# Kernel optimization log

Hardware: AMD Instinct MI355X
Metric: run time of the kernel (lower is better)

Reference implementation:

```python
import jax, jax.numpy as jnp
import numpy as np

N_ITERATIONS = 32
EPS = 1e-8


def setup_inputs() -> dict:
    key = jax.random.key(0)
    k1, k2 = jax.random.split(key)
    x = jax.random.normal(k1, (8, 1, 16384), dtype=jnp.float32)
    # learned dictionary, init uniform(-1, 1) as in the torch module
    d = jax.random.uniform(k2, (512, 1, 512), dtype=jnp.float32, minval=-1.0, maxval=1.0)
    return {"x": x, "d": d}


def reference(x, d):
    B, C, T = x.shape
    n_atoms, _, A = d.shape  # A = atom_size
    # unit_norm over (channels, atom_size) per atom
    dn = d / (jnp.sqrt(jnp.sum(d * d, axis=(1, 2), keepdims=True)) + EPS)
    batch_ids = jnp.arange(B)[:, None]
    offs = jnp.arange(A)[None, :]

    def step(carry, _):
        xr, recon = carry
        xp = jnp.pad(xr, ((0, 0), (0, 0), (0, A)))  # pad right by atom_size
        fm = jax.lax.conv_general_dilated(
            xp, dn, window_strides=(1,), padding='VALID',
            dimension_numbers=('NCH', 'OIH', 'NCH'))[..., :T]  # [B, n_atoms, T]
        flat = fm.reshape(B, n_atoms * T)
        values = jnp.max(flat, axis=-1)            # [B]
        indices = jnp.argmax(flat, axis=-1)        # [B]
        atom_idx = indices // T
        time_idx = indices % T
        atoms = dn[atom_idx] * values[:, None, None]  # [B, C, A]
        pos = time_idx[:, None] + offs                 # [B, A], max < T + A
        end = jnp.clip(time_idx + A, 0, T - 1)         # torch clamps end to T-1
        mask = pos < end[:, None]                      # [B, A]
        vals = jnp.where(mask[:, None, :], atoms, 0.0)  # [B, C, A]
        sp = jnp.zeros((B, C, T + A), xr.dtype)
        # positions are unique per batch item -> scatter-set into padded buffer
        sp = sp.at[batch_ids, :, pos].set(vals.transpose(0, 2, 1))
        sparse = sp[..., :T]
        return (xr - sparse, recon + sparse), None

    (residual, recon), _ = jax.lax.scan(step, (x, jnp.zeros_like(x)), None, length=N_ITERATIONS)
    return residual, recon
```

## Files before the change

### kernel.cpp

```cpp
#include <hip/hip_runtime.h>
#include <cstdint>

#define B_    8
#define T_    16384
#define NA_   512
#define A_    512
#define NIT_  32
#define EPSV  1e-8f

typedef unsigned long long u64;
typedef __attribute__((ext_vector_type(8))) short bf16x8;
typedef __attribute__((ext_vector_type(4))) float f32x4;

union Frag { uint4 u; bf16x8 f; };

#define OFF_INV   0
#define OFF_SELA  512
#define OFF_SELT  768
#define OFF_SELV  1024
#define OFF_CM    1280
#define OFF_RMA   2098432
#define OFF_RMB   2106624
#define OFF_XRA   2114816
#define OFF_XRB   2245888
#define OFF_DPK   2376960
#define MAIN_NEED 2639104
#define OFF_BAR   2639104
#define PERS_NEED (OFF_BAR + 4096)
#define OFF_SXR   OFF_CM
#define OFF_SCAND (OFF_CM + 131072)
#define S_NEED    (OFF_SCAND + 16)

__device__ __forceinline__ unsigned int encf(float f) {
    unsigned int u = __float_as_uint(f);
    return (u & 0x80000000u) ? ~u : (u | 0x80000000u);
}
__device__ __forceinline__ float decf(unsigned int e) {
    unsigned int u = (e & 0x80000000u) ? (e & 0x7fffffffu) : ~e;
    return __uint_as_float(u);
}
__device__ __forceinline__ u64 umax64(u64 a, u64 b) { return a > b ? a : b; }
__device__ __forceinline__ u64 enc64(float v, unsigned int flat) {
    return (((u64)encf(v)) << 32) | (unsigned int)~flat;
}
__device__ __forceinline__ u64 shfl_xor_u64(u64 v, int mask) {
    unsigned int lo = (unsigned int)v, hi = (unsigned int)(v >> 32);
    lo = __shfl_xor(lo, mask, 64);
    hi = __shfl_xor(hi, mask, 64);
    return (((u64)hi) << 32) | lo;
}
__device__ __forceinline__ u64 shfl_down_u64(u64 v, int off) {
    unsigned int lo = (unsigned int)v, hi = (unsigned int)(v >> 32);
    lo = __shfl_down(lo, off, 64);
    hi = __shfl_down(hi, off, 64);
    return (((u64)hi) << 32) | lo;
}
__device__ __forceinline__ unsigned short f2bf(float v) {
    unsigned int u = __float_as_uint(v);
    return (unsigned short)((u + 0x7fffu + ((u >> 16) & 1u)) >> 16);
}
__device__ __forceinline__ unsigned int packhl(float v) {
    unsigned short hb = f2bf(v);
    unsigned short lb = f2bf(v - __uint_as_float((unsigned int)hb << 16));
    return (unsigned int)hb | ((unsigned int)lb << 16);
}

__device__ __forceinline__ float ld_af(const float* p) {
    return __hip_atomic_load(p, __ATOMIC_RELAXED, __HIP_MEMORY_SCOPE_AGENT);
}
__device__ __forceinline__ void st_af(float* p, float v) {
    __hip_atomic_store(p, v, __ATOMIC_RELAXED, __HIP_MEMORY_SCOPE_AGENT);
}
__device__ __forceinline__ u64 ld_au64(const u64* p) {
    return __hip_atomic_load(p, __ATOMIC_RELAXED, __HIP_MEMORY_SCOPE_AGENT);
}
__device__ __forceinline__ void st_au64(u64* p, u64 v) {
    __hip_atomic_store(p, v, __ATOMIC_RELAXED, __HIP_MEMORY_SCOPE_AGENT);
}

__device__ __forceinline__ void b_barrier(unsigned int* slots, int ag, unsigned int gen) {
    __syncthreads();
    const int tid = threadIdx.x;
    if (tid == 0)
        __hip_atomic_store(&slots[ag << 4], gen, __ATOMIC_RELAXED, __HIP_MEMORY_SCOPE_AGENT);
    if (tid < 64) {
        const unsigned int* sp = &slots[(tid & 31) << 4];
        int spins = 0;
        while (__hip_atomic_load(sp, __ATOMIC_RELAXED, __HIP_MEMORY_SCOPE_AGENT) < gen) {
            __builtin_amdgcn_s_sleep(1);
            if (++spins > (1 << 20)) break;
        }
    }
    __syncthreads();
    asm volatile("" ::: "memory");
}

__device__ __forceinline__ void run_super(const uint4* bhp, const uint4* blp,
                                          const uint4* Adl, int sw,
                                          int c0, int tbase, int chbase,
                                          u64* cml, const float* ivv,
                                          int a0, int q, int cl) {
    const int base = c0 << 4;
    f32x4 acc[8];
    const f32x4 zero = {0.f, 0.f, 0.f, 0.f};
    #pragma unroll
    for (int g = 0; g < 8; ++g) acc[g] = zero;

    Frag bh[8], bl[8];
    #pragma unroll
    for (int pp = 0; pp < 8; ++pp) {
        bh[pp].u = bhp[base + 4 * pp];
        bl[pp].u = blp[base + 4 * pp];
    }
    for (int js0 = 0; js0 < 32; js0 += 8) {
        #pragma unroll
        for (int ju = 0; ju < 8; ++ju) {
            const int js = js0 + ju;
            Frag Af;
            Af.u = Adl[(q + 4 * js) ^ sw];
            #pragma unroll
            for (int g = 0; g < 8; ++g)
                acc[g] = __builtin_amdgcn_mfma_f32_16x16x32_bf16(Af.f, bh[(g + ju) & 7].f, acc[g], 0, 0, 0);
            #pragma unroll
            for (int g = 0; g < 8; ++g)
                acc[g] = __builtin_amdgcn_mfma_f32_16x16x32_bf16(Af.f, bl[(g + ju) & 7].f, acc[g], 0, 0, 0);
            bh[ju].u = bhp[base + 4 * (js + 8)];
            bl[ju].u = blp[base + 4 * (js + 8)];
        }
    }
    #pragma unroll
    for (int r = 0; r < 4; ++r) {
        const int atom4 = 4 * q + r;
        const int atom = a0 + atom4;
        u64 m0 = 0ull, m1 = 0ull;
        #pragma unroll
        for (int g = 0; g < 4; ++g) {
            int t = tbase + 64 * c0 + 16 * g + cl;
            m0 = umax64(m0, enc64(acc[g][r] * ivv[r], (unsigned int)(atom * T_ + t)));
        }
        #pragma unroll
        for (int g = 4; g < 8; ++g) {
            int t = tbase + 64 * c0 + 16 * g + cl;
            m1 = umax64(m1, enc64(acc[g][r] * ivv[r], (unsigned int)(atom * T_ + t)));
        }
        m0 = umax64(m0, shfl_xor_u64(m0, 1));
        m0 = umax64(m0, shfl_xor_u64(m0, 2));
        m0 = umax64(m0, shfl_xor_u64(m0, 4));
        m0 = umax64(m0, shfl_xor_u64(m0, 8));
        m1 = umax64(m1, shfl_xor_u64(m1, 1));
        m1 = umax64(m1, shfl_xor_u64(m1, 2));
        m1 = umax64(m1, shfl_xor_u64(m1, 4));
        m1 = umax64(m1, shfl_xor_u64(m1, 8));
        if (cl == 0) {
            cml[(atom4 << 8) + chbase + c0] = m0;
            cml[(atom4 << 8) + chbase + c0 + 1] = m1;
        }
    }
}

__device__ __forceinline__ void run_single(const uint4* bhp, const uint4* blp,
                                           const uint4* Adl, int sw,
                                           int c, int tbase, int chbase,
                                           u64* cml, const float* ivv,
                                           int a0, int q, int cl) {
    const int base = c << 4;
    f32x4 acc[4];
    const f32x4 zero = {0.f, 0.f, 0.f, 0.f};
    #pragma unroll
    for (int g = 0; g < 4; ++g) acc[g] = zero;

    Frag bh[4], bl[4];
    #pragma unroll
    for (int pp = 0; pp < 4; ++pp) {
        bh[pp].u = bhp[base + 4 * pp];
        bl[pp].u = blp[base + 4 * pp];
    }
    for (int js0 = 0; js0 < 32; js0 += 4) {
        #pragma unroll
        for (int ju = 0; ju < 4; ++ju) {
            const int js = js0 + ju;
            Frag Af;
            Af.u = Adl[(q + 4 * js) ^ sw];
            #pragma unroll
            for (int g = 0; g < 4; ++g)
                acc[g] = __builtin_amdgcn_mfma_f32_16x16x32_bf16(Af.f, bh[(g + ju) & 3].f, acc[g], 0, 0, 0);
            #pragma unroll
            for (int g = 0; g < 4; ++g)
                acc[g] = __builtin_amdgcn_mfma_f32_16x16x32_bf16(Af.f, bl[(g + ju) & 3].f, acc[g], 0, 0, 0);
            bh[ju].u = bhp[base + 4 * (js + 4)];
            bl[ju].u = blp[base + 4 * (js + 4)];
        }
    }
    #pragma unroll
    for (int r = 0; r < 4; ++r) {
        const int atom4 = 4 * q + r;
        const int atom = a0 + atom4;
        u64 m0 = 0ull;
        #pragma unroll
        for (int g = 0; g < 4; ++g) {
            int t = tbase + 64 * c + 16 * g + cl;
            m0 = umax64(m0, enc64(acc[g][r] * ivv[r], (unsigned int)(atom * T_ + t)));
        }
        m0 = umax64(m0, shfl_xor_u64(m0, 1));
        m0 = umax64(m0, shfl_xor_u64(m0, 2));
        m0 = umax64(m0, shfl_xor_u64(m0, 4));
        m0 = umax64(m0, shfl_xor_u64(m0, 8));
        if (cl == 0)
            cml[(atom4 << 8) + chbase + c] = m0;
    }
}

__global__ __launch_bounds__(64) void k_inv(const float* __restrict__ d, float* __restrict__ inv,
                                            unsigned int* __restrict__ bar) {
    const int a = blockIdx.x, lane = threadIdx.x;
    if (bar && a == 0) {
        for (int i = lane; i < 4096; i += 64) bar[i] = 0u;
    }
    const float* row = d + a * A_;
    float s = 0.f;
    for (int i = lane; i < A_; i += 64) { float v = row[i]; s = fmaf(v, v, s); }
    #pragma unroll
    for (int o = 32; o > 0; o >>= 1) s += __shfl_down(s, o, 64);
    if (lane == 0) inv[a] = 1.0f / (sqrtf(s) + EPSV);
}

__global__ __launch_bounds__(256) void k_split_d(const float* __restrict__ d,
                                                 unsigned int* __restrict__ dpk) {
    int id = blockIdx.x * 256 + threadIdx.x;
    dpk[id] = packhl(d[id]);
}

__global__ __launch_bounds__(512) void k_persist(const float* __restrict__ x,
                                                 float* __restrict__ xrA,
                                                 float* __restrict__ xrB,
                                                 const float* __restrict__ d,
                                                 const float* __restrict__ inv,
                                                 u64* __restrict__ rmW,
                                                 int* __restrict__ selA,
                                                 int* __restrict__ selT,
                                                 float* __restrict__ selV,
                                                 unsigned int* __restrict__ bar,
                                                 float* __restrict__ out) {
    __shared__ u64 red16[16];
    __shared__ int   selAL[NIT_];
    __shared__ int   selTL[NIT_];
    __shared__ float selVL[NIT_];
    __shared__ uint4 s_hh[4][410];
    __shared__ uint4 s_ll[4][410];
    __shared__ uint4 dl4[16 * 128];
    __shared__ u64  cml[16 * 256];
    const int ag = blockIdx.x, b = blockIdx.y, tid = threadIdx.x;
    const int wave = tid >> 6, lane = tid & 63;
    const int cl = lane & 15, q = lane >> 4;
    const int a0 = ag * 16;
    unsigned int* slots = bar + (b << 9);

    {
        const float4* gsrc = (const float4*)(d + (a0 << 9));
        #pragma unroll
        for (int s = 0; s < 4; ++s) {
            int i = tid + 512 * s;
            int row = i >> 7, c4 = i & 127;
            float4 f = gsrc[i];
            uint4 pk;
            pk.x = packhl(f.x);
            pk.y = packhl(f.y);
            pk.z = packhl(f.z);
            pk.w = packhl(f.w);
            dl4[(row << 7) | (c4 ^ (row & 7))] = pk;
        }
    }

    const uint4* Adl = dl4 + (cl << 7);
    const int sw = cl & 7;
    float ivv[4];
    #pragma unroll
    for (int r = 0; r < 4; ++r) ivv[r] = inv[a0 + 4 * q + r];
    const uint4* bhp = &s_hh[cl & 3][(cl >> 2) + q];
    const uint4* blp = &s_ll[cl & 3][(cl >> 2) + q];
    unsigned int* hw = (unsigned int*)s_hh;
    unsigned int* lw = (unsigned int*)s_ll;

    {
        const float* xb = x + b * T_;
        float cur[4], nxt[4];
        #pragma unroll
        for (int s = 0; s < 4; ++s) {
            const int e = tid + 512 * s;
            cur[s] = (e < 1539) ? xb[e] : 0.f;
        }
        for (int w = 0; w < 16; ++w) {
            const int wb = w << 10;
            if (w) __syncthreads();
            #pragma unroll
            for (int s = 0; s < 4; ++s) {
                const int e = tid + 512 * s;
                if (e < 1539) {
                    float xv = cur[s];
                    unsigned int pw = packhl(xv);
                    unsigned int hword = (pw & 0xffffu) * 0x10001u;
                    unsigned int lword = (pw >> 16) * 0x10001u;
                    #pragma unroll
                    for (int sh = 0; sh < 4; ++sh) {
                        int i = e - sh;
                        if (i >= 0 && i < 1536) { hw[sh * 1640 + i] = hword; lw[sh * 1640 + i] = lword; }
                    }
                }
            }
            __syncthreads();
            if (w + 1 < 16) {
                const int wb2 = (w + 1) << 10;
                #pragma unroll
                for (int s = 0; s < 4; ++s) {
                    const int e = tid + 512 * s;
                    const int t = wb2 + e;
                    nxt[s] = (e < 1539 && t < T_) ? xb[t] : 0.f;
                }
            }
            run_super(bhp, blp, Adl, sw, 2 * wave, wb, w << 4,
                      cml, ivv, a0, q, cl);
            #pragma unroll
            for (int s = 0; s < 4; ++s) cur[s] = nxt[s];
        }
    }
    __syncthreads();

    {
        #pragma unroll
        for (int rr = 0; rr < 2; ++rr) {
            const int rl = wave * 2 + rr;
            const u64* p = cml + (rl << 8);
            u64 m = umax64(umax64(p[lane], p[lane + 64]),
                           umax64(p[lane + 128], p[lane + 192]));
            #pragma unroll
            for (int o = 32; o > 0; o >>= 1) m = umax64(m, shfl_down_u64(m, o));
            if (lane == 0) red16[rl] = m;
        }
        __syncthreads();
        if (wave == 0) {
            u64 wv = (lane < 16) ? red16[lane] : 0ull;
            #pragma unroll
            for (int o = 8; o > 0; o >>= 1) wv = umax64(wv, shfl_xor_u64(wv, o));
            if (lane == 0) st_au64(&rmW[b * 32 + ag], wv);
        }
    }
    unsigned int gen = 1;
    b_barrier(slots, ag, gen); ++gen;

    for (int it = 0; it < NIT_; ++it) {
        const u64* rwp = rmW + ((it & 1) << 8) + b * 32;
        u64 am = ld_au64(&rwp[lane & 31]);
        #pragma unroll
        for (int o = 16; o > 0; o >>= 1) am = umax64(am, shfl_xor_u64(am, o));
        const unsigned int enc = (unsigned int)(am >> 32);
        const unsigned int flat = ~(unsigned int)am;
        const int asel = (int)((flat >> 14) & (NA_ - 1));
        const int tsel = (int)(flat & (T_ - 1));
        const float v = decf(enc);
        if (tid == 0) { selAL[it] = asel; selTL[it] = tsel; selVL[it] = v; }
        if (ag == 0 && tid == 0) {
            selA[it * B_ + b] = asel;
            selT[it * B_ + b] = tsel;
            selV[it * B_ + b] = v;
        }
        if (it == NIT_ - 1) break;
        const int L = min(A_, (T_ - 1) - tsel);
        const float vv = v * inv[asel];

        const float* xrPrev = (it == 0) ? x : ((it & 1) ? xrB : xrA);
        float*       xrNext = (it & 1) ? xrA : xrB;

        int ab = 0, nch = 0, NS = 0;
        float cbuf[4];
        if (L > 0) {
            const int tbeg = max(0, tsel - (A_ - 1));
            const int tend = tsel + L;
            ab = tbeg & ~63;
            const int ae = (tend + 63) & ~63;
            const int W = ae - ab;
            nch = W >> 6;
            NS = W + 512;
            #pragma unroll
            for (int s = 0; s < 4; ++s) {
                const int e = tid + 512 * s;
                const int t = ab + e;
                cbuf[s] = (e < NS + 3 && t < T_) ? ld_af(&xrPrev[b * T_ + t]) : 0.f;
            }
        }

        {
            int t = ag * 512 + tid;
            float xv = ld_af(&xrPrev[b * T_ + t]);
            int o = t - tsel;
            if (L > 0 && o >= 0 && o < L) xv = fmaf(-vv, d[asel * A_ + o], xv);
            st_af(&xrNext[b * T_ + t], xv);
        }

        if (L > 0) {
            #pragma unroll
            for (int s = 0; s < 4; ++s) {
                const int e = tid + 512 * s;
                if (e < NS + 3) {
                    float xv = cbuf[s];
                    int o = (ab + e) - tsel;
                    if (o >= 0 && o < L) xv = fmaf(-vv, d[asel * A_ + o], xv);
                    unsigned int pw = packhl(xv);
                    unsigned int hword = (pw & 0xffffu) * 0x10001u;
                    unsigned int lword = (pw >> 16) * 0x10001u;
                    #pragma unroll
                    for (int sh = 0; sh < 4; ++sh) {
                        int i = e - sh;
                        if (i >= 0 && i < NS) { hw[sh * 1640 + i] = hword; lw[sh * 1640 + i] = lword; }
                    }
                }
            }
            __syncthreads();

            {
                const int lo = (wave * nch) >> 3;
                const int hi = ((wave + 1) * nch) >> 3;
                int c = lo;
                for (; c + 1 < hi; c += 2)
                    run_super(bhp, blp, Adl, sw, c, ab, ab >> 6,
                              cml, ivv, a0, q, cl);
                if (c < hi)
                    run_single(bhp, blp, Adl, sw, c, ab, ab >> 6,
                               cml, ivv, a0, q, cl);
            }
            __syncthreads();
        }

        #pragma unroll
        for (int rr = 0; rr < 2; ++rr) {
            const int rl = wave * 2 + rr;
            const u64* p = cml + (rl << 8);
            u64 m = umax64(umax64(p[lane], p[lane + 64]),
                           umax64(p[lane + 128], p[lane + 192]));
            #pragma unroll
            for (int o = 32; o > 0; o >>= 1) m = umax64(m, shfl_down_u64(m, o));
            if (lane == 0) red16[rl] = m;
        }
        __syncthreads();
        if (wave == 0) {
            u64 wv = (lane < 16) ? red16[lane] : 0ull;
            #pragma unroll
            for (int o = 8; o > 0; o >>= 1) wv = umax64(wv, shfl_xor_u64(wv, o));
            if (lane == 0) st_au64(&rmW[(((it + 1) & 1) << 8) + b * 32 + ag], wv);
        }

        b_barrier(slots, ag, gen); ++gen;
    }

    __syncthreads();
    {
        const int t = ag * 512 + tid;
        const int gid = b * T_ + t;
        float r = x[gid];
        float rec = 0.f;
        for (int k = 0; k < NIT_; ++k) {
            int a  = selAL[k] & (NA_ - 1);
            int ts = selTL[k] & (T_ - 1);
            float vvl = selVL[k] * inv[a];
            int o = t - ts;
            int Lf = min(A_, (T_ - 1) - ts);
            if (o >= 0 && o < Lf) {
                float c = vvl * d[a * A_ + o];
                r -= c;
                rec += c;
            }
        }
        out[gid] = r;
        out[B_ * T_ + gid] = rec;
    }
}


__global__ __launch_bounds__(512) void k_conv(const float* __restrict__ x,
                                              const unsigned int* __restrict__ dpk,
                                              const float* __restrict__ inv,
                                              u64* __restrict__ cm,
                                              float* __restrict__ xrA) {
    __shared__ uint4 s_hh[4][202];
    __shared__ uint4 s_ll[4][202];
    const int tid = threadIdx.x;
    const int wave = tid >> 6, lane = tid & 63;
    const int cl = lane & 15, q = lane >> 4;
    const int wb = blockIdx.x * 256;
    const int gb = blockIdx.z;

    unsigned int* hw = (unsigned int*)s_hh;
    unsigned int* lw = (unsigned int*)s_ll;
    for (int e = tid; e < 776; e += 512) {
        int t = wb + e;
        float xv = (t < T_) ? x[gb * T_ + t] : 0.f;
        if (blockIdx.y == 0 && e < 256) xrA[gb * T_ + wb + e] = xv;
        unsigned int pw = packhl(xv);
        unsigned int hword = (pw & 0xffffu) * 0x10001u;
        unsigned int lword = (pw >> 16) * 0x10001u;
        #pragma unroll
        for (int s = 0; s < 4; ++s) {
            int i = e - s;
            if (i >= 0 && i < 772) { hw[s * 808 + i] = hword; lw[s * 808 + i] = lword; }
        }
    }
    __syncthreads();

    const int a_base = blockIdx.y * 128 + (wave & 1) * 64;
    const int t0l = (wave >> 1) * 64;
    const unsigned int* Ap[4];
    #pragma unroll
    for (int at = 0; at < 4; ++at)
        Ap[at] = dpk + ((a_base + 16 * at + cl) << 9) + 4 * q;
    const uint4* bhp = &s_hh[cl & 3][(t0l >> 2) + (cl >> 2) + q];
    const uint4* blp = &s_ll[cl & 3][(t0l >> 2) + (cl >> 2) + q];

    f32x4 acc[4][4];
    const f32x4 zero = {0.f, 0.f, 0.f, 0.f};
    #pragma unroll
    for (int at = 0; at < 4; ++at)
        #pragma unroll
        for (int tt = 0; tt < 4; ++tt) acc[at][tt] = zero;

    for (int j0 = 0; j0 < A_; j0 += 16) {
        Frag Af[4], bh[4], bl[4];
        #pragma unroll
        for (int at = 0; at < 4; ++at) Af[at].u = *(const uint4*)(Ap[at] + j0);
        #pragma unroll
        for (int tt = 0; tt < 4; ++tt) {
            bh[tt].u = bhp[4 * tt + (j0 >> 2)];
            bl[tt].u = blp[4 * tt + (j0 >> 2)];
        }
        #pragma unroll
        for (int tt = 0; tt < 4; ++tt)
            #pragma unroll
            for (int at = 0; at < 4; ++at)
                acc[at][tt] = __builtin_amdgcn_mfma_f32_16x16x32_bf16(Af[at].f, bh[tt].f, acc[at][tt], 0, 0, 0);
        #pragma unroll
        for (int tt = 0; tt < 4; ++tt)
            #pragma unroll
            for (int at = 0; at < 4; ++at)
                acc[at][tt] = __builtin_amdgcn_mfma_f32_16x16x32_bf16(Af[at].f, bl[tt].f, acc[at][tt], 0, 0, 0);
    }

    const int t0 = wb + t0l;
    const int ch = t0 >> 6;
    #pragma unroll
    for (int at = 0; at < 4; ++at) {
        #pragma unroll
        for (int r = 0; r < 4; ++r) {
            const int atom = a_base + 16 * at + 4 * q + r;
            const float iv = inv[atom];
            u64 m = 0ull;
            #pragma unroll
            for (int tt = 0; tt < 4; ++tt) {
                int t = t0 + 16 * tt + cl;
                m = umax64(m, enc64(acc[at][tt][r] * iv, (unsigned int)(atom * T_ + t)));
            }
            m = umax64(m, shfl_xor_u64(m, 1));
            m = umax64(m, shfl_xor_u64(m, 2));
            m = umax64(m, shfl_xor_u64(m, 4));
            m = umax64(m, shfl_xor_u64(m, 8));
            if (cl == 0)
                cm[((size_t)(gb * NA_ + atom) << 8) + ch] = m;
        }
    }
}

__global__ __launch_bounds__(256) void k_tables(const u64* __restrict__ cm, u64* __restrict__ rm) {
    const int row = blockIdx.x * 4 + (threadIdx.x >> 6);
    const int lane = threadIdx.x & 63;
    const u64* p = cm + ((size_t)row << 8);
    u64 m = 0ull;
    #pragma unroll
    for (int k = 0; k < 4; ++k) m = umax64(m, p[lane + 64 * k]);
    #pragma unroll
    for (int o = 32; o > 0; o >>= 1) m = umax64(m, shfl_down_u64(m, o));
    if (lane == 0) rm[row] = m;
}

__global__ __launch_bounds__(512) void k_it(const float* __restrict__ xrPrev,
                                            float* __restrict__ xrNext,
                                            const float* __restrict__ d,
                                            const float* __restrict__ inv,
                                            const unsigned int* __restrict__ dpk,
                                            u64* __restrict__ cm,
                                            const u64* __restrict__ rmPrev,
                                            u64* __restrict__ rmNext,
                                            int* __restrict__ selA,
                                            int* __restrict__ selT,
                                            float* __restrict__ selV,
                                            int it) {
    __shared__ u64 red8[8];
    __shared__ uint4 s_hh[4][410];
    __shared__ uint4 s_ll[4][410];
    __shared__ uint4 dl4[16 * 128];
    const int ag = blockIdx.x, b = blockIdx.y, tid = threadIdx.x;
    const int wave = tid >> 6, lane = tid & 63;
    const int cl = lane & 15, q = lane >> 4;
    const int a0 = ag * 16;

    {
        const uint4* gsrc = (const uint4*)(dpk + (a0 << 9));
        #pragma unroll
        for (int s = 0; s < 4; ++s) {
            int i = tid + 512 * s;
            int row = i >> 7, c4 = i & 127;
            dl4[(row << 7) | (c4 ^ (row & 7))] = gsrc[i];
        }
    }

    const u64* rp = rmPrev + b * NA_;
    u64 am = rp[tid];
    #pragma unroll
    for (int o = 32; o > 0; o >>= 1) am = umax64(am, shfl_xor_u64(am, o));
    if (lane == 0) red8[wave] = am;
    __syncthreads();
    u64 win = red8[0];
    #pragma unroll
    for (int w2 = 1; w2 < 8; ++w2) win = umax64(win, red8[w2]);
    const unsigned int enc = (unsigned int)(win >> 32);
    const unsigned int flat = ~(unsigned int)win;
    const int asel = (int)((flat >> 14) & (NA_ - 1));
    const int tsel = (int)(flat & (T_ - 1));
    const float v = decf(enc);
    if (ag == 0 && tid == 0) {
        selA[it * B_ + b] = asel;
        selT[it * B_ + b] = tsel;
        selV[it * B_ + b] = v;
    }
    const int L = min(A_, (T_ - 1) - tsel);
    const float vv = v * inv[asel];

    {
        int t = ag * 512 + tid;
        float xv = xrPrev[b * T_ + t];
        int o = t - tsel;
        if (L > 0 && o >= 0 && o < L) xv = fmaf(-vv, d[asel * A_ + o], xv);
        xrNext[b * T_ + t] = xv;
    }

    if (L > 0) {
        const int tbeg = max(0, tsel - (A_ - 1));
        const int tend = tsel + L;
        const int ab = tbeg & ~63;
        const int ae = (tend + 63) & ~63;
        const int W = ae - ab;
        const int nch = W >> 6;
        const int NS = W + 512;

        unsigned int* hw = (unsigned int*)s_hh;
        unsigned int* lw = (unsigned int*)s_ll;
        for (int e = tid; e < NS + 3; e += 512) {
            int t = ab + e;
            float xv = (t < T_) ? xrPrev[b * T_ + t] : 0.f;
            int o = t - tsel;
            if (o >= 0 && o < L) xv = fmaf(-vv, d[asel * A_ + o], xv);
            unsigned int pw = packhl(xv);
            unsigned int hword = (pw & 0xffffu) * 0x10001u;
            unsigned int lword = (pw >> 16) * 0x10001u;
            #pragma unroll
            for (int s = 0; s < 4; ++s) {
                int i = e - s;
                if (i >= 0 && i < NS) { hw[s * 1640 + i] = hword; lw[s * 1640 + i] = lword; }
            }
        }
        __syncthreads();

        const uint4* Adl = dl4 + (cl << 7);
        const int sw = cl & 7;
        float ivv[4];
        #pragma unroll
        for (int r = 0; r < 4; ++r) ivv[r] = inv[a0 + 4 * q + r];
        const uint4* bhp = &s_hh[cl & 3][(cl >> 2) + q];
        const uint4* blp = &s_ll[cl & 3][(cl >> 2) + q];

        for (int c = wave; c < nch; c += 8) {
            f32x4 acc[4];
            const f32x4 zero = {0.f, 0.f, 0.f, 0.f};
            #pragma unroll
            for (int tt = 0; tt < 4; ++tt) acc[tt] = zero;

            Frag bh[4], bl[4];
            #pragma unroll
            for (int pp = 0; pp < 4; ++pp) {
                bh[pp].u = bhp[16 * c + 4 * pp];
                bl[pp].u = blp[16 * c + 4 * pp];
            }
            for (int j0 = 0; j0 < A_; j0 += 64) {
                #pragma unroll
                for (int u = 0; u < 4; ++u) {
                    const int jj = j0 + 16 * u;
                    Frag Af;
                    Af.u = Adl[(q + (jj >> 2)) ^ sw];
                    #pragma unroll
                    for (int tt = 0; tt < 4; ++tt)
                        acc[tt] = __builtin_amdgcn_mfma_f32_16x16x32_bf16(Af.f, bh[(u + tt) & 3].f, acc[tt], 0, 0, 0);
                    #pragma unroll
                    for (int tt = 0; tt < 4; ++tt)
                        acc[tt] = __builtin_amdgcn_mfma_f32_16x16x32_bf16(Af.f, bl[(u + tt) & 3].f, acc[tt], 0, 0, 0);
                    bh[u].u = bhp[16 * c + (jj >> 2) + 16];
                    bl[u].u = blp[16 * c + (jj >> 2) + 16];
                }
            }
            #pragma unroll
            for (int r = 0; r < 4; ++r) {
                const int atom = a0 + 4 * q + r;
                u64 mm = 0ull;
                #pragma unroll
                for (int tt = 0; tt < 4; ++tt) {
                    int t = ab + 64 * c + 16 * tt + cl;
                    mm = umax64(mm, enc64(acc[tt][r] * ivv[r], (unsigned int)(atom * T_ + t)));
                }
                mm = umax64(mm, shfl_xor_u64(mm, 1));
                mm = umax64(mm, shfl_xor_u64(mm, 2));
                mm = umax64(mm, shfl_xor_u64(mm, 4));
                mm = umax64(mm, shfl_xor_u64(mm, 8));
                if (cl == 0)
                    cm[((size_t)(b * NA_ + atom) << 8) + (ab >> 6) + c] = mm;
            }
        }
        __syncthreads();
    }

    #pragma unroll
    for (int rr = 0; rr < 2; ++rr) {
        const int row = a0 + wave * 2 + rr;
        const u64* p = cm + ((size_t)(b * NA_ + row) << 8);
        u64 m = umax64(umax64(p[lane], p[lane + 64]),
                       umax64(p[lane + 128], p[lane + 192]));
        #pragma unroll
        for (int o = 32; o > 0; o >>= 1) m = umax64(m, shfl_down_u64(m, o));
        if (lane == 0) rmNext[b * NA_ + row] = m;
    }
}

__global__ void s_init(const float* __restrict__ x, float* __restrict__ xr,
                       u64* __restrict__ cand) {
    int i = blockIdx.x * 256 + threadIdx.x;
    if (i < B_ * T_) xr[i] = x[i];
    if (i < B_) cand[i] = 0ull;
}
__global__ __launch_bounds__(256) void s_scan(const float* __restrict__ xr,
                                              const float* __restrict__ d,
                                              const float* __restrict__ inv,
                                              u64* __restrict__ cand) {
    __shared__ float dLs[A_];
    __shared__ u64 redU[256];
    const int aB = blockIdx.x, b = blockIdx.y, tid = threadIdx.x;
    const float iv = inv[aB];
    for (int i = tid; i < A_; i += 256) dLs[i] = d[aB * A_ + i] * iv;
    __syncthreads();
    const float* xb = xr + b * T_;
    u64 best = 0ull;
    for (int t = tid; t < T_; t += 256) {
        float acc = 0.f;
        int lim = min(A_, T_ - t);
        for (int i = 0; i < lim; ++i) acc = fmaf(dLs[i], xb[t + i], acc);
        best = umax64(best, enc64(acc, (unsigned int)(aB * T_ + t)));
    }
    redU[tid] = best;
    __syncthreads();
    for (int s = 128; s > 0; s >>= 1) {
        if (tid < s) redU[tid] = umax64(redU[tid], redU[tid + s]);
        __syncthreads();
    }
    if (tid == 0) atomicMax(&cand[b], redU[0]);
}
__global__ void s_apply(float* __restrict__ xr, const float* __restrict__ d,
                        const float* __restrict__ inv, u64* __restrict__ cand,
                        int* selA, int* selT, float* selV, int it) {
    const int b = blockIdx.x, tid = threadIdx.x;
    u64 win = cand[b];
    unsigned int enc = (unsigned int)(win >> 32);
    unsigned int flat = ~(unsigned int)win;
    int a = (int)((flat >> 14) & (NA_ - 1)), t = (int)(flat & (T_ - 1));
    float v = decf(enc);
    if (tid == 0) { selA[it * B_ + b] = a; selT[it * B_ + b] = t; selV[it * B_ + b] = v; }
    float vvl = v * inv[a];
    int L = min(A_, (T_ - 1) - t);
    for (int o = tid; o < L; o += 256) xr[b * T_ + t + o] -= vvl * d[a * A_ + o];
    if (tid == 0) cand[b] = 0ull;
}

__global__ __launch_bounds__(256) void k_final(const float* __restrict__ x,
                                               const float* __restrict__ d,
                                               const int* __restrict__ selA,
                                               const int* __restrict__ selT,
                                               const float* __restrict__ selV,
                                               const float* __restrict__ inv,
                                               float* __restrict__ out) {
    const int gid = blockIdx.x * 256 + threadIdx.x;
    const int b = gid >> 14;
    const int t = gid & (T_ - 1);
    float r = x[gid];
    float rec = 0.f;
    for (int k = 0; k < NIT_; ++k) {
        int a  = selA[k * B_ + b] & (NA_ - 1);
        int ts = selT[k * B_ + b] & (T_ - 1);
        float vvl = selV[k * B_ + b] * inv[a];
        int o = t - ts;
        int L = min(A_, (T_ - 1) - ts);
        if (o >= 0 && o < L) {
            float c = vvl * d[a * A_ + o];
            r -= c;
            rec += c;
        }
    }
    out[gid] = r;
    out[B_ * T_ + gid] = rec;
}

extern "C" void kernel_launch(void* const* d_in, const int* in_sizes, int n_in,
                              void* d_out, int out_size, void* d_ws, size_t ws_size,
                              hipStream_t stream) {
    const float* x = (const float*)d_in[0];
    const float* d = (const float*)d_in[1];
    float* out = (float*)d_out;
    float* ws = (float*)d_ws;
    const size_t wsf = ws_size / sizeof(float);

    float* inv  = ws + OFF_INV;
    int*   selA = (int*)(ws + OFF_SELA);
    int*   selT = (int*)(ws + OFF_SELT);
    float* selV = ws + OFF_SELV;

    if (wsf < (size_t)S_NEED) return;

    const bool persistOK = wsf >= (size_t)PERS_NEED;
    unsigned int* bar = persistOK ? (unsigned int*)(ws + OFF_BAR) : (unsigned int*)0;

    k_inv<<<dim3(NA_), dim3(64), 0, stream>>>(d, inv, bar);

    if (wsf >= (size_t)MAIN_NEED) {
        u64* cm  = (u64*)(ws + OFF_CM);
        u64* rmA = (u64*)(ws + OFF_RMA);
        u64* rmB = (u64*)(ws + OFF_RMB);
        float* xrA = ws + OFF_XRA;
        float* xrB = ws + OFF_XRB;
        unsigned int* dpk = (unsigned int*)(ws + OFF_DPK);

        if (persistOK) {
            u64* rmW = (u64*)(ws + OFF_RMA);
            k_persist<<<dim3(NA_ / 16, B_), dim3(512), 0, stream>>>(x, xrA, xrB, d, inv,
                                                                    rmW, selA, selT, selV,
                                                                    bar, out);
            return;
        }

        k_split_d<<<dim3(NA_ * A_ / 256), dim3(256), 0, stream>>>(d, dpk);
        k_conv<<<dim3(T_ / 256, NA_ / 128, B_), dim3(512), 0, stream>>>(x, dpk, inv, cm, xrA);
        k_tables<<<dim3(B_ * NA_ / 4), dim3(256), 0, stream>>>(cm, rmA);
        for (int it = 0; it < NIT_; ++it) {
            const float* xp = (it & 1) ? xrB : xrA;
            float*       xn = (it & 1) ? xrA : xrB;
            const u64*   ro = (it & 1) ? rmB : rmA;
            u64*         rn = (it & 1) ? rmA : rmB;
            k_it<<<dim3(NA_ / 16, B_), dim3(512), 0, stream>>>(xp, xn, d, inv, dpk,
                                                               cm, ro, rn,
                                                               selA, selT, selV, it);
        }
    } else {
        float* xr = ws + OFF_SXR;
        u64* cand = (u64*)(ws + OFF_SCAND);
        s_init<<<dim3((B_ * T_ + 255) / 256), dim3(256), 0, stream>>>(x, xr, cand);
        for (int it = 0; it < NIT_; ++it) {
            s_scan<<<dim3(NA_, B_), dim3(256), 0, stream>>>(xr, d, inv, cand);
            s_apply<<<dim3(B_), dim3(256), 0, stream>>>(xr, d, inv, cand, selA, selT, selV, it);
        }
    }

    k_final<<<dim3(B_ * T_ / 256), dim3(256), 0, stream>>>(x, d, selA, selT, selV, inv, out);
}
```

Measured before the change: 811.2 us.

## Skip dictionary-low term in persistent correlation using separate high-part atom layout

In the persistent kernel's run_super and run_single, the second MFMA pass over the signal's low bf16 residual now multiplies only the dictionary's high bf16 part. It uses a compact half-K layout: a new ah4 shared array packs only the high halves of the dictionary, and an lp buffer holds just the signal's low halves, loaded as K=32 pairs. This roughly halves the MFMA work and LDS traffic of the low-part correction term. It drops the tiny low×low cross product, slightly changing numerics, and adds shared-memory layout complexity plus scalar 32-bit LDS loads that may cause bank conflicts.

Measured after the change: 706.4 us. 1.15x faster.

```diff
diff --git a/kernel.cpp b/kernel.cpp
--- a/kernel.cpp
+++ b/kernel.cpp
@@ -13,6 +13,8 @@
 typedef __attribute__((ext_vector_type(4))) float f32x4;
 
 union Frag { uint4 u; bf16x8 f; };
+
+#define MFMA16(a, b, c) __builtin_amdgcn_mfma_f32_16x16x32_bf16((a), (b), (c), 0, 0, 0)
 
 #define OFF_INV   0
 #define OFF_SELA  512
@@ -95,8 +97,17 @@
     asm volatile("" ::: "memory");
 }
 
-__device__ __forceinline__ void run_super(const uint4* bhp, const uint4* blp,
+__device__ __forceinline__ uint4 lp4(const unsigned int* lps, int w) {
+    uint4 r;
+    r.x = lps[w]; r.y = lps[w + 1]; r.z = lps[w + 2]; r.w = lps[w + 3];
+    return r;
+}
+
+
+__device__ __forceinline__ void run_super(const uint4* bhp,
                                           const uint4* Adl, int sw,
+                                          const unsigned int* lps,
+                                          const uint4* A2p,
                                           int c0, int tbase, int chbase,
                                           u64* cml, const float* ivv,
                                           int a0, int q, int cl) {
@@ -106,26 +117,40 @@
     #pragma unroll
     for (int g = 0; g < 8; ++g) acc[g] = zero;
 
-    Frag bh[8], bl[8];
-    #pragma unroll
-    for (int pp = 0; pp < 8; ++pp) {
-        bh[pp].u = bhp[base + 4 * pp];
-        bl[pp].u = blp[base + 4 * pp];
-    }
-    for (int js0 = 0; js0 < 32; js0 += 8) {
-        #pragma unroll
-        for (int ju = 0; ju < 8; ++ju) {
-            const int js = js0 + ju;
-            Frag Af;
-            Af.u = Adl[(q + 4 * js) ^ sw];
-            #pragma unroll
-            for (int g = 0; g < 8; ++g)
-                acc[g] = __builtin_amdgcn_mfma_f32_16x16x32_bf16(Af.f, bh[(g + ju) & 7].f, acc[g], 0, 0, 0);
-            #pragma unroll
-            for (int g = 0; g < 8; ++g)
-                acc[g] = __builtin_amdgcn_mfma_f32_16x16x32_bf16(Af.f, bl[(g + ju) & 7].f, acc[g], 0, 0, 0);
-            bh[ju].u = bhp[base + 4 * (js + 8)];
-            bl[ju].u = blp[base + 4 * (js + 8)];
+    {
+        Frag bh[8];
+        #pragma unroll
+        for (int pp = 0; pp < 8; ++pp) bh[pp].u = bhp[base + 4 * pp];
+        for (int js0 = 0; js0 < 32; js0 += 8) {
+            #pragma unroll
+            for (int ju = 0; ju < 8; ++ju) {
+                const int js = js0 + ju;
+                Frag Af;
+                Af.u = Adl[(q + 4 * js) ^ sw];
+                #pragma unroll
+                for (int g = 0; g < 8; ++g)
+                    acc[g] = MFMA16(Af.f, bh[(g + ju) & 7].f, acc[g]);
+                bh[ju].u = bhp[base + 4 * (js + 8)];
+            }
+        }
+    }
+    {
+        const int bb = 32 * c0 + 4 * q + (cl >> 1);
+        Frag b2[8];
+        #pragma unroll
+        for (int m = 0; m < 8; ++m) b2[m].u = lp4(lps, bb + 8 * m);
+        for (int j2b = 0; j2b < 4; ++j2b) {
+            #pragma unroll
+            for (int j2u = 0; j2u < 4; ++j2u) {
+                const int j2 = 4 * j2b + j2u;
+                Frag A2;
+                A2.u = A2p[(4 * j2 + q) ^ sw];
+                #pragma unroll
+                for (int g = 0; g < 8; ++g)
+                    acc[g] = MFMA16(A2.f, b2[(g + 2 * j2u) & 7].f, acc[g]);
+                b2[(2 * j2u) & 7].u     = lp4(lps, bb + 8 * (2 * j2 + 8));
+                b2[(2 * j2u + 1) & 7].u = lp4(lps, bb + 8 * (2 * j2 + 9));
+            }
         }
     }
     #pragma unroll
@@ -158,8 +183,10 @@
     }
 }
 
-__device__ __forceinline__ void run_single(const uint4* bhp, const uint4* blp,
+__device__ __forceinline__ void run_single(const uint4* bhp,
                                            const uint4* Adl, int sw,
+                                           const unsigned int* lps,
+                                           const uint4* A2p,
                                            int c, int tbase, int chbase,
                                            u64* cml, const float* ivv,
                                            int a0, int q, int cl) {
@@ -169,26 +196,40 @@
     #pragma unroll
     for (int g = 0; g < 4; ++g) acc[g] = zero;
 
-    Frag bh[4], bl[4];
-    #pragma unroll
-    for (int pp = 0; pp < 4; ++pp) {
-        bh[pp].u = bhp[base + 4 * pp];
-        bl[pp].u = blp[base + 4 * pp];
-    }
-    for (int js0 = 0; js0 < 32; js0 += 4) {
-        #pragma unroll
-        for (int ju = 0; ju < 4; ++ju) {
-            const int js = js0 + ju;
-            Frag Af;
-            Af.u = Adl[(q + 4 * js) ^ sw];
-            #pragma unroll
-            for (int g = 0; g < 4; ++g)
-                acc[g] = __builtin_amdgcn_mfma_f32_16x16x32_bf16(Af.f, bh[(g + ju) & 3].f, acc[g], 0, 0, 0);
-            #pragma unroll
-            for (int g = 0; g < 4; ++g)
-                acc[g] = __builtin_amdgcn_mfma_f32_16x16x32_bf16(Af.f, bl[(g + ju) & 3].f, acc[g], 0, 0, 0);
-            bh[ju].u = bhp[base + 4 * (js + 4)];
-            bl[ju].u = blp[base + 4 * (js + 4)];
+    {
+        Frag bh[4];
+        #pragma unroll
+        for (int pp = 0; pp < 4; ++pp) bh[pp].u = bhp[base + 4 * pp];
+        for (int js0 = 0; js0 < 32; js0 += 4) {
+            #pragma unroll
+            for (int ju = 0; ju < 4; ++ju) {
+                const int js = js0 + ju;
+                Frag Af;
+                Af.u = Adl[(q + 4 * js) ^ sw];
+                #pragma unroll
+                for (int g = 0; g < 4; ++g)
+                    acc[g] = MFMA16(Af.f, bh[(g + ju) & 3].f, acc[g]);
+                bh[ju].u = bhp[base + 4 * (js + 4)];
+            }
+        }
+    }
+    {
+        const int bb = 32 * c + 4 * q + (cl >> 1);
+        Frag b2[4];
+        #pragma unroll
+        for (int m = 0; m < 4; ++m) b2[m].u = lp4(lps, bb + 8 * m);
+        for (int j2b = 0; j2b < 8; ++j2b) {
+            #pragma unroll
+            for (int j2u = 0; j2u < 2; ++j2u) {
+                const int j2 = 2 * j2b + j2u;
+                Frag A2;
+                A2.u = A2p[(4 * j2 + q) ^ sw];
+                #pragma unroll
+                for (int g = 0; g < 4; ++g)
+                    acc[g] = MFMA16(A2.f, b2[(g + 2 * j2u) & 3].f, acc[g]);
+                b2[(2 * j2u) & 3].u     = lp4(lps, bb + 8 * (2 * j2 + 4));
+                b2[(2 * j2u + 1) & 3].u = lp4(lps, bb + 8 * (2 * j2 + 5));
+            }
         }
     }
     #pragma unroll
@@ -246,7 +287,8 @@
     __shared__ int   selTL[NIT_];
     __shared__ float selVL[NIT_];
     __shared__ uint4 s_hh[4][410];
-    __shared__ uint4 s_ll[4][410];
+    __shared__ unsigned int lp[2][816];
+    __shared__ uint4 ah4[16 * 64];
     __shared__ uint4 dl4[16 * 128];
     __shared__ u64  cml[16 * 256];
     const int ag = blockIdx.x, b = blockIdx.y, tid = threadIdx.x;
@@ -254,9 +296,12 @@
     const int cl = lane & 15, q = lane >> 4;
     const int a0 = ag * 16;
     unsigned int* slots = bar + (b << 9);
+    unsigned short* lp0s = (unsigned short*)&lp[0][0];
+    unsigned short* lp1s = (unsigned short*)&lp[1][0];
 
     {
         const float4* gsrc = (const float4*)(d + (a0 << 9));
+        unsigned int* ah32 = (unsigned int*)ah4;
         #pragma unroll
         for (int s = 0; s < 4; ++s) {
             int i = tid + 512 * s;
@@ -268,18 +313,25 @@
             pk.z = packhl(f.z);
             pk.w = packhl(f.w);
             dl4[(row << 7) | (c4 ^ (row & 7))] = pk;
+            unsigned int d0 = (pk.x & 0xffffu) | ((pk.y & 0xffffu) << 16);
+            unsigned int d1 = (pk.z & 0xffffu) | ((pk.w & 0xffffu) << 16);
+            int u = c4 >> 1;
+            int l0 = (2 * c4) & 3;
+            int abase = (row << 8) + ((u ^ (row & 7)) << 2);
+            ah32[abase + l0] = d0;
+            ah32[abase + l0 + 1] = d1;
         }
     }
 
     const uint4* Adl = dl4 + (cl << 7);
+    const uint4* A2p = ah4 + (cl << 6);
     const int sw = cl & 7;
+    const unsigned int* lps = &lp[cl & 1][0];
     float ivv[4];
     #pragma unroll
     for (int r = 0; r < 4; ++r) ivv[r] = inv[a0 + 4 * q + r];
     const uint4* bhp = &s_hh[cl & 3][(cl >> 2) + q];
-    const uint4* blp = &s_ll[cl & 3][(cl >> 2) + q];
     unsigned int* hw = (unsigned int*)s_hh;
-    unsigned int* lw = (unsigned int*)s_ll;
 
     {
         const float* xb = x + b * T_;
@@ -296,15 +348,16 @@
             for (int s = 0; s < 4; ++s) {
                 const int e = tid + 512 * s;
                 if (e < 1539) {
-                    float xv = cur[s];
-                    unsigned int pw = packhl(xv);
+                    unsigned int pw = packhl(cur[s]);
                     unsigned int hword = (pw & 0xffffu) * 0x10001u;
-                    unsigned int lword = (pw >> 16) * 0x10001u;
                     #pragma unroll
                     for (int sh = 0; sh < 4; ++sh) {
                         int i = e - sh;
-                        if (i >= 0 && i < 1536) { hw[sh * 1640 + i] = hword; lw[sh * 1640 + i] = lword; }
+                        if (i >= 0 && i < 1536) hw[sh * 1640 + i] = hword;
                     }
+                    unsigned short lo = (unsigned short)(pw >> 16);
+                    lp0s[e] = lo;
+                    if (e > 0) lp1s[e - 1] = lo;
                 }
             }
             __syncthreads();
@@ -317,7 +370,7 @@
                     nxt[s] = (e < 1539 && t < T_) ? xb[t] : 0.f;
                 }
             }
-            run_super(bhp, blp, Adl, sw, 2 * wave, wb, w << 4,
+            run_super(bhp, Adl, sw, lps, A2p, 2 * wave, wb, w << 4,
                       cml, ivv, a0, q, cl);
             #pragma unroll
             for (int s = 0; s < 4; ++s) cur[s] = nxt[s];
@@ -406,12 +459,14 @@
                     if (o >= 0 && o < L) xv = fmaf(-vv, d[asel * A_ + o], xv);
                     unsigned int pw = packhl(xv);
                     unsigned int hword = (pw & 0xffffu) * 0x10001u;
-                    unsigned int lword = (pw >> 16) * 0x10001u;
                     #pragma unroll
                     for (int sh = 0; sh < 4; ++sh) {
                         int i = e - sh;
-                        if (i >= 0 && i < NS) { hw[sh * 1640 + i] = hword; lw[sh * 1640 + i] = lword; }
+                        if (i >= 0 && i < NS) hw[sh * 1640 + i] = hword;
                     }
+                    unsigned short lo = (unsigned short)(pw >> 16);
+                    lp0s[e] = lo;
+                    if (e > 0) lp1s[e - 1] = lo;
                 }
             }
             __syncthreads();
@@ -421,10 +476,10 @@
                 const int hi = ((wave + 1) * nch) >> 3;
                 int c = lo;
                 for (; c + 1 < hi; c += 2)
-                    run_super(bhp, blp, Adl, sw, c, ab, ab >> 6,
+                    run_super(bhp, Adl, sw, lps, A2p, c, ab, ab >> 6,
                               cml, ivv, a0, q, cl);
                 if (c < hi)
-                    run_single(bhp, blp, Adl, sw, c, ab, ab >> 6,
+                    run_single(bhp, Adl, sw, lps, A2p, c, ab, ab >> 6,
                                cml, ivv, a0, q, cl);
             }
             __syncthreads();
@@ -534,12 +589,12 @@
         for (int tt = 0; tt < 4; ++tt)
             #pragma unroll
             for (int at = 0; at < 4; ++at)
-                acc[at][tt] = __builtin_amdgcn_mfma_f32_16x16x32_bf16(Af[at].f, bh[tt].f, acc[at][tt], 0, 0, 0);
+                acc[at][tt] = MFMA16(Af[at].f, bh[tt].f, acc[at][tt]);
         #pragma unroll
         for (int tt = 0; tt < 4; ++tt)
             #pragma unroll
             for (int at = 0; at < 4; ++at)
-                acc[at][tt] = __builtin_amdgcn_mfma_f32_16x16x32_bf16(Af[at].f, bl[tt].f, acc[at][tt], 0, 0, 0);
+                acc[at][tt] = MFMA16(Af[at].f, bl[tt].f, acc[at][tt]);
     }
 
     const int t0 = wb + t0l;
@@ -694,10 +749,10 @@
                     Af.u = Adl[(q + (jj >> 2)) ^ sw];
                     #pragma unroll
                     for (int tt = 0; tt < 4; ++tt)
-                        acc[tt] = __builtin_amdgcn_mfma_f32_16x16x32_bf16(Af.f, bh[(u + tt) & 3].f, acc[tt], 0, 0, 0);
+                        acc[tt] = MFMA16(Af.f, bh[(u + tt) & 3].f, acc[tt]);
                     #pragma unroll
                     for (int tt = 0; tt < 4; ++tt)
-                        acc[tt] = __builtin_amdgcn_mfma_f32_16x16x32_bf16(Af.f, bl[(u + tt) & 3].f, acc[tt], 0, 0, 0);
+                        acc[tt] = MFMA16(Af.f, bl[(u + tt) & 3].f, acc[tt]);
                     bh[u].u = bhp[16 * c + (jj >> 2) + 16];
                     bl[u].u = blp[16 * c + (jj >> 2) + 16];
                 }
```
